# Kernel tuning notes

Hardware: AMD Instinct MI355X
Metric: run time of the kernel (lower is better)

Reference implementation:

```python
import jax, jax.numpy as jnp
import numpy as np

EMBED = 256; G = 8; NC = 6; NL = 4; NP = 13
BS = 1; NA = 900
IMG_W, IMG_H = 704.0, 256.0
LEVEL_HW = [(64, 176), (32, 88), (16, 44), (8, 22)]


def setup_inputs() -> dict:
    key = jax.random.key(0)
    ks = jax.random.split(key, 12)
    inp = {}
    inp["instance_feature"] = jax.random.normal(ks[0], (BS, NA, EMBED), jnp.float32)
    inp["anchor_embed"] = jax.random.normal(ks[1], (BS, NA, EMBED), jnp.float32)
    # key points in normalized [0,1) cube; projection matrix maps them to pixel coords
    inp["key_points"] = jax.random.uniform(ks[2], (BS, NA, NP, 3), jnp.float32)
    for i, (h, w) in enumerate(LEVEL_HW):
        inp[f"fm{i}"] = jax.random.normal(ks[3 + i], (BS, NC, EMBED, h, w), jnp.float32)
    # intrinsics-like projection: x->x*W, y->y*H, depth ~ z+0.5, plus per-camera jitter
    base = jnp.array([[IMG_W, 0.0, 0.0, 0.0],
                      [0.0, IMG_H, 0.0, 0.0],
                      [0.0, 0.0, 1.0, 0.5],
                      [0.0, 0.0, 0.0, 1.0]], jnp.float32)
    inp["projection_mat"] = base[None, None] + 0.05 * jax.random.normal(ks[7], (BS, NC, 4, 4), jnp.float32)
    inp["image_wh"] = jnp.broadcast_to(jnp.array([IMG_W, IMG_H], jnp.float32), (BS, NC, 2))
    inp["w_weights"] = 0.02 * jax.random.normal(ks[8], (EMBED, G * NC * NL * NP), jnp.float32)
    inp["b_weights"] = jnp.zeros((G * NC * NL * NP,), jnp.float32)
    inp["w_out"] = 0.02 * jax.random.normal(ks[9], (EMBED, EMBED), jnp.float32)
    inp["b_out"] = jnp.zeros((EMBED,), jnp.float32)
    return inp


def _grid_sample(fm, grid):
    # fm: (B, C, H, W); grid: (B, A, P, 2) in [-1,1]. Bilinear, zero padding,
    # align_corners=False (torch F.grid_sample defaults). Returns (B, A, P, C).
    B, C, H, W = fm.shape
    A, P = grid.shape[1], grid.shape[2]
    gx = (grid[..., 0] + 1.0) * (W * 0.5) - 0.5
    gy = (grid[..., 1] + 1.0) * (H * 0.5) - 0.5
    x0 = jnp.floor(gx); y0 = jnp.floor(gy)
    fmf = jnp.transpose(fm.reshape(B, C, H * W), (0, 2, 1))  # (B, HW, C)

    def gather(xi, yi):
        valid = (xi >= 0) & (xi <= W - 1) & (yi >= 0) & (yi <= H - 1)
        xc = jnp.clip(xi, 0, W - 1).astype(jnp.int32)
        yc = jnp.clip(yi, 0, H - 1).astype(jnp.int32)
        idx = (yc * W + xc).reshape(B, A * P, 1)
        g = jnp.take_along_axis(fmf, idx, axis=1).reshape(B, A, P, C)
        return g * valid[..., None].astype(fm.dtype)

    wx1 = gx - x0; wx0 = 1.0 - wx1
    wy1 = gy - y0; wy0 = 1.0 - wy1
    return (gather(x0, y0) * (wx0 * wy0)[..., None]
            + gather(x0 + 1.0, y0) * (wx1 * wy0)[..., None]
            + gather(x0, y0 + 1.0) * (wx0 * wy1)[..., None]
            + gather(x0 + 1.0, y0 + 1.0) * (wx1 * wy1)[..., None])


def reference(instance_feature, anchor_embed, key_points, fm0, fm1, fm2, fm3,
              projection_mat, image_wh, w_weights, b_weights, w_out, b_out):
    bs, na = instance_feature.shape[:2]
    gd = EMBED // G
    # _get_weights: softmax over (cams*levels*pts) jointly, per group
    feat = instance_feature + anchor_embed
    w = (feat @ w_weights + b_weights).reshape(bs, na, NC * NL * NP, G)
    w = jax.nn.softmax(w, axis=2).reshape(bs, na, NC, NL, NP, G)
    # feature_sampling: project 3D key points to each camera's pixel plane
    kp_h = jnp.concatenate([key_points, jnp.ones_like(key_points[..., :1])], axis=-1)
    p2 = jnp.einsum('bcij,banj->bcani', projection_mat, kp_h)  # (bs,cams,na,pts,4)
    xy = p2[..., :2] / jnp.maximum(p2[..., 2:3], 1e-5)
    grid = (xy / image_wh[:, :, None, None]) * 2.0 - 1.0
    grid = grid.reshape(bs * NC, na, NP, 2)
    # bilinear sample every pyramid level for every camera
    feats = jnp.stack([
        _grid_sample(fm.reshape(bs * NC, EMBED, fm.shape[-2], fm.shape[-1]), grid)
        for fm in (fm0, fm1, fm2, fm3)
    ], axis=0)  # (L, bs*cams, na, pts, E)
    feats = feats.reshape(NL, bs, NC, na, NP, G, gd)
    # multi_view_level_fusion: weighted sum over cams and levels, per group
    fused = jnp.einsum('baclpg,lbcapgd->bapgd', w, feats).reshape(bs, na, NP, EMBED)
    out = fused.sum(axis=2)  # sum over key points
    return out @ w_out + b_out + instance_feature  # output_proj + residual 'add'
```

## Files before the change

kernel.cpp:

```cpp
#include <hip/hip_runtime.h>
#include <hip/hip_bf16.h>
#include <hip/hip_fp16.h>
#include <cstdint>

#define EMBED 256
#define GPS 8
#define NCAM 6
#define NLVL 4
#define NPT 13
#define NANC 900
#define NSAMP (NCAM*NLVL*NPT)
#define NWCOL (GPS*NSAMP)
#define MPAD 928
#define WSTRIDE 328
#define MAXENT 320

#define FMOFF0 0
#define FMOFF1 17301504
#define FMOFF2 21626880
#define FMOFF3 22708224
#define TALL_ELEMS 22978560

typedef __attribute__((ext_vector_type(8))) short bf16x8;
typedef __attribute__((ext_vector_type(16))) float f32x16;
typedef __attribute__((ext_vector_type(8))) unsigned short ushort8_t;

__device__ __forceinline__ ushort bf16bits(float x) {
    __hip_bfloat16 h = __float2bfloat16(x);
    return *reinterpret_cast<ushort*>(&h);
}
__device__ __forceinline__ ushort h16bits(float x) {
    __half h = __float2half(x);
    return *reinterpret_cast<ushort*>(&h);
}
__device__ __forceinline__ __half2 u2h2(unsigned u) {
    union { unsigned u; __half2 h; } cv; cv.u = u; return cv.h;
}

__global__ __launch_bounds__(256) void k_prep(
        const float* __restrict__ fm0, const float* __restrict__ fm1,
        const float* __restrict__ fm2, const float* __restrict__ fm3,
        __half* __restrict__ t0, __half* __restrict__ t1,
        __half* __restrict__ t2, __half* __restrict__ t3,
        const float* __restrict__ wlin, __hip_bfloat16* __restrict__ wt,
        const float* __restrict__ inst, const float* __restrict__ anch,
        __hip_bfloat16* __restrict__ featB,
        const float* __restrict__ kp, const float* __restrict__ proj,
        float* __restrict__ pxy) {
    __shared__ ushort lds2[256 * 64];
    int b = blockIdx.x;
    int t = threadIdx.x;
    if (b < 1404) {
        const float* in; __half* outp; int HW, chunks, lb;
        if (b < 1056)      { in = fm0; outp = t0; HW = 11264; chunks = 176; lb = b; }
        else if (b < 1320) { in = fm1; outp = t1; HW = 2816;  chunks = 44;  lb = b - 1056; }
        else if (b < 1386) { in = fm2; outp = t2; HW = 704;   chunks = 11;  lb = b - 1320; }
        else               { in = fm3; outp = t3; HW = 176;   chunks = 3;   lb = b - 1386; }
        int c = lb / chunks;
        int hw0 = (lb - c * chunks) * 64;
        int q = t & 15, eg = t >> 4;
        bool vld = (hw0 + q * 4 + 3) < HW;
        const float* srcq = in + (size_t)c * EMBED * HW + hw0 + q * 4;
        float4 vals[16];
        #pragma unroll
        for (int r = 0; r < 16; r++) {
            int e = eg + r * 16;
            vals[r] = vld ? *(const float4*)(srcq + (size_t)e * HW)
                          : make_float4(0.f, 0.f, 0.f, 0.f);
        }
        #pragma unroll
        for (int r = 0; r < 16; r++) {
            int e = eg + r * 16;
            int sw = ((e >> 3) & 15) * 4;
            ushort4 u;
            u.x = h16bits(vals[r].x); u.y = h16bits(vals[r].y);
            u.z = h16bits(vals[r].z); u.w = h16bits(vals[r].w);
            *reinterpret_cast<ushort4*>(&lds2[e * 64 + ((q * 4) ^ sw)]) = u;
        }
        __syncthreads();
        ushort* outb = reinterpret_cast<ushort*>(outp) + ((size_t)c * HW + hw0) * EMBED;
        #pragma unroll
        for (int r = 0; r < 8; r++) {
            int flat = r * 2048 + t * 8;
            int hw = flat >> 8;
            int e0 = flat & 255;
            if (hw0 + hw < HW) {
                ushort8_t u;
                #pragma unroll
                for (int j = 0; j < 8; j++) {
                    int e = e0 + j;
                    int sw = ((e >> 3) & 15) * 4;
                    u[j] = lds2[e * 64 + (hw ^ sw)];
                }
                *reinterpret_cast<ushort8_t*>(outb + flat) = u;
            }
        }
    } else if (b < 1560) {
        int b1 = b - 1404;
        int kt = b1 / 39, nt = b1 - kt * 39;
        int k0 = kt * 64, n0 = nt * 64;
        int grp = t >> 6, nn = t & 63;
        #pragma unroll
        for (int r = 0; r < 16; r++) {
            int kk = grp * 16 + r;
            lds2[kk * 65 + nn] = bf16bits(wlin[(size_t)(k0 + kk) * NWCOL + n0 + nn]);
        }
        __syncthreads();
        ushort* wtb = reinterpret_cast<ushort*>(wt);
        int kk2 = t & 63;
        #pragma unroll
        for (int r = 0; r < 16; r++) {
            int nn2 = grp * 16 + r;
            wtb[(size_t)(n0 + nn2) * EMBED + k0 + kk2] = lds2[kk2 * 65 + nn2];
        }
    } else if (b < 1785) {
        int base = (b - 1560) * 1024 + t * 4;
        float4 a = *(const float4*)&inst[base];
        float4 c = *(const float4*)&anch[base];
        ushort4 r;
        r.x = bf16bits(a.x + c.x); r.y = bf16bits(a.y + c.y);
        r.z = bf16bits(a.z + c.z); r.w = bf16bits(a.w + c.w);
        *reinterpret_cast<ushort4*>(reinterpret_cast<ushort*>(featB) + base) = r;
    } else if (b < 1792) {
        int base = 900 * EMBED + (b - 1785) * 1024 + t * 4;
        ushort4 z; z.x = z.y = z.z = z.w = 0;
        *reinterpret_cast<ushort4*>(reinterpret_cast<ushort*>(featB) + base) = z;
    } else {
        int i = (b - 1792) * 256 + t;
        if (i < NANC * NCAM * NPT) {
            int a = i / (NCAM * NPT);
            int r = i - a * (NCAM * NPT);
            int c = r / NPT;
            int p = r - c * NPT;
            const float* M = proj + c * 16;
            const float* k3 = kp + ((size_t)a * NPT + p) * 3;
            float kx = k3[0], ky = k3[1], kz = k3[2];
            float X = M[0] * kx + M[1] * ky + M[2] * kz + M[3];
            float Y = M[4] * kx + M[5] * ky + M[6] * kz + M[7];
            float Z = M[8] * kx + M[9] * ky + M[10] * kz + M[11];
            float invz = 1.f / fmaxf(Z, 1e-5f);
            pxy[(size_t)i * 2 + 0] = X * invz;
            pxy[(size_t)i * 2 + 1] = Y * invz;
        }
    }
}

#define MT 29
#define NT 78
__global__ __launch_bounds__(256) void k_gemm(const __hip_bfloat16* __restrict__ featB,
                                              const __hip_bfloat16* __restrict__ wt,
                                              const float* __restrict__ blin,
                                              float* __restrict__ logits) {
    int wv = threadIdx.x >> 6, lane = threadIdx.x & 63;
    int idx = blockIdx.x * 4 + wv;
    if (idx >= MT * NT) return;
    int mt = idx % MT, nt = idx / MT;
    int m0 = mt * 32, n0 = nt * 32;
    int l31 = lane & 31;
    int khalf = (lane >> 5) * 8;
    const short* ap = reinterpret_cast<const short*>(featB) + (size_t)(m0 + l31) * EMBED + khalf;
    const short* bp = reinterpret_cast<const short*>(wt)    + (size_t)(n0 + l31) * EMBED + khalf;
    f32x16 acc = {};
    #pragma unroll 8
    for (int ki = 0; ki < 16; ki++) {
        bf16x8 a = *reinterpret_cast<const bf16x8*>(ap + ki * 16);
        bf16x8 bb = *reinterpret_cast<const bf16x8*>(bp + ki * 16);
        acc = __builtin_amdgcn_mfma_f32_32x32x16_bf16(a, bb, acc, 0, 0, 0);
    }
    float bias = blin[n0 + l31];
    int colg = n0 + l31;
    #pragma unroll
    for (int r = 0; r < 16; r++) {
        int row = (r & 3) + 8 * (r >> 2) + 4 * (lane >> 5);
        int grow = m0 + row;
        if (grow < NANC)
            logits[(size_t)grow * NWCOL + colg] = acc[r] + bias;
    }
}

__global__ __launch_bounds__(512) void k_aggregate(const __half* __restrict__ tAll,
                                                   const float* __restrict__ logits,
                                                   const float* __restrict__ pxy,
                                                   const float* __restrict__ wout,
                                                   const float* __restrict__ bout,
                                                   const float* __restrict__ inst,
                                                   float* __restrict__ out) {
    __shared__ float wT[GPS * WSTRIDE];
    __shared__ float xyS[NCAM * NPT * 2];
    __shared__ float redS[8][EMBED];
    __shared__ float pS[EMBED];
    __shared__ int4  eOff[MAXENT];
    __shared__ float4 eW[MAXENT];
    __shared__ int   eS[MAXENT];
    __shared__ int   cntS;
    int a = blockIdx.x;
    int tid = threadIdx.x;
    int wave = tid >> 6;
    int lane = tid & 63;
    if (tid == 0) cntS = 0;
    for (int j = tid; j < NWCOL; j += 512)
        wT[(j & 7) * WSTRIDE + (j >> 3)] = logits[(size_t)a * NWCOL + j];
    for (int j = tid; j < NCAM * NPT * 2; j += 512)
        xyS[j] = pxy[(size_t)a * NCAM * NPT * 2 + j];
    __syncthreads();
    {
        int g = wave;
        float m = -1e30f;
        for (int s = lane; s < NSAMP; s += 64) m = fmaxf(m, wT[g * WSTRIDE + s]);
        #pragma unroll
        for (int off = 32; off; off >>= 1) m = fmaxf(m, __shfl_xor(m, off));
        float ssum = 0.f;
        for (int s = lane; s < NSAMP; s += 64) ssum += __expf(wT[g * WSTRIDE + s] - m);
        #pragma unroll
        for (int off = 32; off; off >>= 1) ssum += __shfl_xor(ssum, off);
        float rs = 1.f / ssum;
        for (int s = lane; s < NSAMP; s += 64)
            wT[g * WSTRIDE + s] = __expf(wT[g * WSTRIDE + s] - m) * rs;
    }
    {
        bool valid = false; int4 o4; float4 w4;
        if (tid < NSAMP) {
            int c = tid / 52, rem = tid - c * 52;
            int l = rem / 13, p = rem - l * 13;
            float X = xyS[(c * NPT + p) * 2], Y = xyS[(c * NPT + p) * 2 + 1];
            int Wl = 176 >> l, Hl = 64 >> l;
            float scale = 0.25f / (float)(1 << l);
            float gx = fmaf(X, scale, -0.5f);
            float gy = fmaf(Y, scale, -0.5f);
            float x0f = floorf(gx), y0f = floorf(gy);
            float fx = gx - x0f, fy = gy - y0f;
            int x0 = (int)x0f, y0 = (int)y0f;
            int x1 = x0 + 1, y1 = y0 + 1;
            bool vx0 = (x0 >= 0) && (x0 < Wl);
            bool vx1 = (x1 >= 0) && (x1 < Wl);
            bool vy0 = (y0 >= 0) && (y0 < Hl);
            bool vy1 = (y1 >= 0) && (y1 < Hl);
            w4.x = (vx0 && vy0) ? (1.f - fx) * (1.f - fy) : 0.f;
            w4.y = (vx1 && vy0) ? fx * (1.f - fy) : 0.f;
            w4.z = (vx0 && vy1) ? (1.f - fx) * fy : 0.f;
            w4.w = (vx1 && vy1) ? fx * fy : 0.f;
            if (w4.x + w4.y + w4.z + w4.w > 0.f) {
                valid = true;
                int xc0 = min(max(x0, 0), Wl - 1), xc1 = min(max(x1, 0), Wl - 1);
                int yc0 = min(max(y0, 0), Hl - 1), yc1 = min(max(y1, 0), Hl - 1);
                const int lvlBase[4] = { FMOFF0, FMOFF1, FMOFF2, FMOFF3 };
                int cb = lvlBase[l] + c * (Wl * Hl) * EMBED;
                o4.x = cb + (yc0 * Wl + xc0) * EMBED;
                o4.y = cb + (yc0 * Wl + xc1) * EMBED;
                o4.z = cb + (yc1 * Wl + xc0) * EMBED;
                o4.w = cb + (yc1 * Wl + xc1) * EMBED;
            }
        }
        unsigned long long mask = __ballot(valid);
        int prefix = __popcll(mask & ((1ull << lane) - 1ull));
        int wcount = __popcll(mask);
        int basev = 0;
        if (lane == 0 && wcount) basev = atomicAdd(&cntS, wcount);
        basev = __shfl(basev, 0);
        if (valid) {
            int pos = basev + prefix;
            eOff[pos] = o4; eW[pos] = w4; eS[pos] = tid;
        }
    }
    __syncthreads();
    int cnt = cntS;
    int cnt_pad = (cnt + 15) & ~15;
    for (int j = cnt + tid; j < cnt_pad; j += 512) {
        eOff[j] = make_int4(0, 0, 0, 0);
        eW[j] = make_float4(0.f, 0.f, 0.f, 0.f);
        eS[j] = 0;
    }
    __syncthreads();
    int e0 = lane * 4;
    int g = lane >> 3;
    float a0 = 0.f, a1 = 0.f, a2 = 0.f, a3 = 0.f;
    auto consume = [&](const float4& w, int sIdx,
                       uint2 l0, uint2 l1, uint2 l2, uint2 l3) {
        float wg = wT[g * WSTRIDE + sIdx];
        __half2 W00 = __float2half2_rn(w.x), W01 = __float2half2_rn(w.y);
        __half2 W10 = __float2half2_rn(w.z), W11 = __float2half2_rn(w.w);
        __half2 blo = __hfma2(u2h2(l0.x), W00,
                      __hfma2(u2h2(l1.x), W01,
                      __hfma2(u2h2(l2.x), W10,
                      __hmul2(u2h2(l3.x), W11))));
        __half2 bhi = __hfma2(u2h2(l0.y), W00,
                      __hfma2(u2h2(l1.y), W01,
                      __hfma2(u2h2(l2.y), W10,
                      __hmul2(u2h2(l3.y), W11))));
        float2 flo = __half22float2(blo);
        float2 fhi = __half22float2(bhi);
        a0 = fmaf(wg, flo.x, a0);
        a1 = fmaf(wg, flo.y, a1);
        a2 = fmaf(wg, fhi.x, a2);
        a3 = fmaf(wg, fhi.y, a3);
    };
    int per = cnt_pad >> 3;
    if (per > 0) {
        int idx = wave;
        int4 oA = eOff[idx]; float4 wA = eW[idx]; int sA = eS[idx];
        uint2 vA0 = *(const uint2*)(tAll + oA.x + e0);
        uint2 vA1 = *(const uint2*)(tAll + oA.y + e0);
        uint2 vA2 = *(const uint2*)(tAll + oA.z + e0);
        uint2 vA3 = *(const uint2*)(tAll + oA.w + e0);
        for (int it = 0; it < per; it += 2) {
            int j = idx + 8;
            int4 oB = eOff[j]; float4 wB = eW[j]; int sB = eS[j];
            uint2 vB0 = *(const uint2*)(tAll + oB.x + e0);
            uint2 vB1 = *(const uint2*)(tAll + oB.y + e0);
            uint2 vB2 = *(const uint2*)(tAll + oB.z + e0);
            uint2 vB3 = *(const uint2*)(tAll + oB.w + e0);
            consume(wA, sA, vA0, vA1, vA2, vA3);
            idx = j + 8;
            if (it + 2 < per) {
                oA = eOff[idx]; wA = eW[idx]; sA = eS[idx];
                vA0 = *(const uint2*)(tAll + oA.x + e0);
                vA1 = *(const uint2*)(tAll + oA.y + e0);
                vA2 = *(const uint2*)(tAll + oA.z + e0);
                vA3 = *(const uint2*)(tAll + oA.w + e0);
            }
            consume(wB, sB, vB0, vB1, vB2, vB3);
        }
    }
    redS[wave][e0 + 0] = a0; redS[wave][e0 + 1] = a1;
    redS[wave][e0 + 2] = a2; redS[wave][e0 + 3] = a3;
    __syncthreads();
    int col = tid & 255;
    int kh = tid >> 8;
    if (kh == 0) {
        float s = redS[0][col] + redS[1][col] + redS[2][col] + redS[3][col]
                + redS[4][col] + redS[5][col] + redS[6][col] + redS[7][col];
        redS[0][col] = s;
    }
    __syncthreads();
    float acc = 0.f;
    int kbase = kh * 128;
    #pragma unroll 8
    for (int k = 0; k < 128; k++)
        acc = fmaf(redS[0][kbase + k], wout[(size_t)(kbase + k) * EMBED + col], acc);
    if (kh == 1) pS[col] = acc;
    __syncthreads();
    if (kh == 0)
        out[(size_t)a * EMBED + col] = acc + pS[col] + bout[col] + inst[(size_t)a * EMBED + col];
}

extern "C" void kernel_launch(void* const* d_in, const int* in_sizes, int n_in,
                              void* d_out, int out_size, void* d_ws, size_t ws_size,
                              hipStream_t stream) {
    const float* inst = (const float*)d_in[0];
    const float* anch = (const float*)d_in[1];
    const float* kp   = (const float*)d_in[2];
    const float* fm0  = (const float*)d_in[3];
    const float* fm1  = (const float*)d_in[4];
    const float* fm2  = (const float*)d_in[5];
    const float* fm3  = (const float*)d_in[6];
    const float* proj = (const float*)d_in[7];
    const float* wlin = (const float*)d_in[9];
    const float* blin = (const float*)d_in[10];
    const float* wout = (const float*)d_in[11];
    const float* bout = (const float*)d_in[12];
    float* out = (float*)d_out;

    char* ws = (char*)d_ws;
    size_t off = 0;
    auto alloc = [&](size_t bytes) -> void* {
        void* p = ws + off;
        off = (off + bytes + 255) & ~(size_t)255;
        return p;
    };
    __half* tAll = (__half*)alloc((size_t)TALL_ELEMS * 2);
    __half* t0 = tAll + FMOFF0;
    __half* t1 = tAll + FMOFF1;
    __half* t2 = tAll + FMOFF2;
    __half* t3 = tAll + FMOFF3;
    __hip_bfloat16* wt    = (__hip_bfloat16*)alloc((size_t)NWCOL * EMBED * 2);
    __hip_bfloat16* featB = (__hip_bfloat16*)alloc((size_t)MPAD * EMBED * 2);
    float* logits = (float*)alloc((size_t)NANC * NWCOL * 4);
    float* pxy    = (float*)alloc((size_t)NANC * NCAM * NPT * 2 * 4);

    k_prep<<<dim3(2067), 256, 0, stream>>>(fm0, fm1, fm2, fm3, t0, t1, t2, t3,
                                           wlin, wt, inst, anch, featB, kp, proj, pxy);
    k_gemm<<<dim3((MT * NT + 3) / 4), 256, 0, stream>>>(featB, wt, blin, logits);
    k_aggregate<<<dim3(NANC), 512, 0, stream>>>(tAll, logits, pxy,
                                                wout, bout, inst, out);
}
```

Baseline: 217.1 us.

## Store transposed feature maps as FP8 instead of FP16

The prep kernel now packs each channel-last feature map element into FP8 (e4m3 via cvt_pk_fp8) instead of half precision, halving the transposed buffer size. The aggregate kernel loads 4 bytes per lane per corner and unpacks them to fp32 with cvt_pk_f32_fp8, then folds the bilinear and softmax weights in fp32. The aim is to cut global write traffic in prep and gather bandwidth in aggregate. The cost is a large loss of precision in the sampled features, which may hurt accuracy against a float32 reference, plus a changed LDS swizzle and larger entry padding.

```diff
diff --git a/kernel.cpp b/kernel.cpp
--- a/kernel.cpp
+++ b/kernel.cpp
@@ -13,45 +13,38 @@
 #define NWCOL (GPS*NSAMP)
 #define MPAD 928
 #define WSTRIDE 328
-#define MAXENT 320
+#define MAXENT 352
 
 #define FMOFF0 0
 #define FMOFF1 17301504
 #define FMOFF2 21626880
 #define FMOFF3 22708224
-#define TALL_ELEMS 22978560
+#define TALL_BYTES 22978560
 
 typedef __attribute__((ext_vector_type(8))) short bf16x8;
 typedef __attribute__((ext_vector_type(16))) float f32x16;
-typedef __attribute__((ext_vector_type(8))) unsigned short ushort8_t;
+typedef __attribute__((ext_vector_type(2))) float v2f;
 
 __device__ __forceinline__ ushort bf16bits(float x) {
     __hip_bfloat16 h = __float2bfloat16(x);
     return *reinterpret_cast<ushort*>(&h);
 }
-__device__ __forceinline__ ushort h16bits(float x) {
-    __half h = __float2half(x);
-    return *reinterpret_cast<ushort*>(&h);
-}
-__device__ __forceinline__ __half2 u2h2(unsigned u) {
-    union { unsigned u; __half2 h; } cv; cv.u = u; return cv.h;
-}
 
 __global__ __launch_bounds__(256) void k_prep(
         const float* __restrict__ fm0, const float* __restrict__ fm1,
         const float* __restrict__ fm2, const float* __restrict__ fm3,
-        __half* __restrict__ t0, __half* __restrict__ t1,
-        __half* __restrict__ t2, __half* __restrict__ t3,
+        unsigned char* __restrict__ t0, unsigned char* __restrict__ t1,
+        unsigned char* __restrict__ t2, unsigned char* __restrict__ t3,
         const float* __restrict__ wlin, __hip_bfloat16* __restrict__ wt,
         const float* __restrict__ inst, const float* __restrict__ anch,
         __hip_bfloat16* __restrict__ featB,
         const float* __restrict__ kp, const float* __restrict__ proj,
         float* __restrict__ pxy) {
-    __shared__ ushort lds2[256 * 64];
+    __shared__ ushort lds2[128 * 64];
     int b = blockIdx.x;
     int t = threadIdx.x;
     if (b < 1404) {
-        const float* in; __half* outp; int HW, chunks, lb;
+        const float* in; unsigned char* outp; int HW, chunks, lb;
         if (b < 1056)      { in = fm0; outp = t0; HW = 11264; chunks = 176; lb = b; }
         else if (b < 1320) { in = fm1; outp = t1; HW = 2816;  chunks = 44;  lb = b - 1056; }
         else if (b < 1386) { in = fm2; outp = t2; HW = 704;   chunks = 11;  lb = b - 1320; }
@@ -64,35 +57,40 @@
         float4 vals[16];
         #pragma unroll
         for (int r = 0; r < 16; r++) {
-            int e = eg + r * 16;
+            int e = 2 * eg + (r & 1) + 32 * (r >> 1);
             vals[r] = vld ? *(const float4*)(srcq + (size_t)e * HW)
                           : make_float4(0.f, 0.f, 0.f, 0.f);
         }
         #pragma unroll
-        for (int r = 0; r < 16; r++) {
-            int e = eg + r * 16;
-            int sw = ((e >> 3) & 15) * 4;
-            ushort4 u;
-            u.x = h16bits(vals[r].x); u.y = h16bits(vals[r].y);
-            u.z = h16bits(vals[r].z); u.w = h16bits(vals[r].w);
-            *reinterpret_cast<ushort4*>(&lds2[e * 64 + ((q * 4) ^ sw)]) = u;
+        for (int rp = 0; rp < 8; rp++) {
+            int ep = eg + 16 * rp;
+            int s2 = (ep >> 1) & 62;
+            float4 va = vals[2 * rp], vb = vals[2 * rp + 1];
+            uint p0 = (uint)__builtin_amdgcn_cvt_pk_fp8_f32(va.x, vb.x, 0, false) & 0xffff;
+            uint p1 = (uint)__builtin_amdgcn_cvt_pk_fp8_f32(va.y, vb.y, 0, false) & 0xffff;
+            uint p2 = (uint)__builtin_amdgcn_cvt_pk_fp8_f32(va.z, vb.z, 0, false) & 0xffff;
+            uint p3 = (uint)__builtin_amdgcn_cvt_pk_fp8_f32(va.w, vb.w, 0, false) & 0xffff;
+            int col01 = (q * 4) ^ s2;
+            int col23 = (q * 4 + 2) ^ s2;
+            *reinterpret_cast<uint*>(&lds2[ep * 64 + col01]) = p0 | (p1 << 16);
+            *reinterpret_cast<uint*>(&lds2[ep * 64 + col23]) = p2 | (p3 << 16);
         }
         __syncthreads();
-        ushort* outb = reinterpret_cast<ushort*>(outp) + ((size_t)c * HW + hw0) * EMBED;
+        ushort* outb = reinterpret_cast<ushort*>(outp) + ((size_t)c * HW + hw0) * 128;
         #pragma unroll
         for (int r = 0; r < 8; r++) {
             int flat = r * 2048 + t * 8;
             int hw = flat >> 8;
-            int e0 = flat & 255;
+            int ep0 = (flat & 255) >> 1;
             if (hw0 + hw < HW) {
-                ushort8_t u;
+                ushort4 u;
                 #pragma unroll
-                for (int j = 0; j < 8; j++) {
-                    int e = e0 + j;
-                    int sw = ((e >> 3) & 15) * 4;
-                    u[j] = lds2[e * 64 + (hw ^ sw)];
+                for (int j = 0; j < 4; j++) {
+                    int ep = ep0 + j;
+                    int s2 = (ep >> 1) & 62;
+                    u[j] = lds2[ep * 64 + (hw ^ s2)];
                 }
-                *reinterpret_cast<ushort8_t*>(outb + flat) = u;
+                *reinterpret_cast<ushort4*>(outb + flat / 2) = u;
             }
         }
     } else if (b < 1560) {
@@ -178,7 +176,7 @@
     }
 }
 
-__global__ __launch_bounds__(512) void k_aggregate(const __half* __restrict__ tAll,
+__global__ __launch_bounds__(512) void k_aggregate(const unsigned char* __restrict__ tAll,
                                                    const float* __restrict__ logits,
                                                    const float* __restrict__ pxy,
                                                    const float* __restrict__ wout,
@@ -265,7 +263,7 @@
     __syncthreads();
     int cnt = cntS;
     int cnt_pad = (cnt + 15) & ~15;
-    for (int j = cnt + tid; j < cnt_pad; j += 512) {
+    for (int j = cnt + tid; j < cnt_pad + 16; j += 512) {
         eOff[j] = make_int4(0, 0, 0, 0);
         eW[j] = make_float4(0.f, 0.f, 0.f, 0.f);
         eS[j] = 0;
@@ -275,48 +273,45 @@
     int g = lane >> 3;
     float a0 = 0.f, a1 = 0.f, a2 = 0.f, a3 = 0.f;
     auto consume = [&](const float4& w, int sIdx,
-                       uint2 l0, uint2 l1, uint2 l2, uint2 l3) {
+                       uint c00, uint c01, uint c10, uint c11) {
         float wg = wT[g * WSTRIDE + sIdx];
-        __half2 W00 = __float2half2_rn(w.x), W01 = __float2half2_rn(w.y);
-        __half2 W10 = __float2half2_rn(w.z), W11 = __float2half2_rn(w.w);
-        __half2 blo = __hfma2(u2h2(l0.x), W00,
-                      __hfma2(u2h2(l1.x), W01,
-                      __hfma2(u2h2(l2.x), W10,
-                      __hmul2(u2h2(l3.x), W11))));
-        __half2 bhi = __hfma2(u2h2(l0.y), W00,
-                      __hfma2(u2h2(l1.y), W01,
-                      __hfma2(u2h2(l2.y), W10,
-                      __hmul2(u2h2(l3.y), W11))));
-        float2 flo = __half22float2(blo);
-        float2 fhi = __half22float2(bhi);
-        a0 = fmaf(wg, flo.x, a0);
-        a1 = fmaf(wg, flo.y, a1);
-        a2 = fmaf(wg, fhi.x, a2);
-        a3 = fmaf(wg, fhi.y, a3);
+        float wwx = wg * w.x, wwy = wg * w.y, wwz = wg * w.z, www = wg * w.w;
+        v2f l00 = __builtin_amdgcn_cvt_pk_f32_fp8(c00, false);
+        v2f h00 = __builtin_amdgcn_cvt_pk_f32_fp8(c00, true);
+        v2f l01 = __builtin_amdgcn_cvt_pk_f32_fp8(c01, false);
+        v2f h01 = __builtin_amdgcn_cvt_pk_f32_fp8(c01, true);
+        v2f l10 = __builtin_amdgcn_cvt_pk_f32_fp8(c10, false);
+        v2f h10 = __builtin_amdgcn_cvt_pk_f32_fp8(c10, true);
+        v2f l11 = __builtin_amdgcn_cvt_pk_f32_fp8(c11, false);
+        v2f h11 = __builtin_amdgcn_cvt_pk_f32_fp8(c11, true);
+        a0 = fmaf(wwx, l00.x, fmaf(wwy, l01.x, fmaf(wwz, l10.x, fmaf(www, l11.x, a0))));
+        a1 = fmaf(wwx, l00.y, fmaf(wwy, l01.y, fmaf(wwz, l10.y, fmaf(www, l11.y, a1))));
+        a2 = fmaf(wwx, h00.x, fmaf(wwy, h01.x, fmaf(wwz, h10.x, fmaf(www, h11.x, a2))));
+        a3 = fmaf(wwx, h00.y, fmaf(wwy, h01.y, fmaf(wwz, h10.y, fmaf(www, h11.y, a3))));
     };
     int per = cnt_pad >> 3;
     if (per > 0) {
         int idx = wave;
         int4 oA = eOff[idx]; float4 wA = eW[idx]; int sA = eS[idx];
-        uint2 vA0 = *(const uint2*)(tAll + oA.x + e0);
-        uint2 vA1 = *(const uint2*)(tAll + oA.y + e0);
-        uint2 vA2 = *(const uint2*)(tAll + oA.z + e0);
-        uint2 vA3 = *(const uint2*)(tAll + oA.w + e0);
+        uint vA0 = *(const uint*)(tAll + oA.x + e0);
+        uint vA1 = *(const uint*)(tAll + oA.y + e0);
+        uint vA2 = *(const uint*)(tAll + oA.z + e0);
+        uint vA3 = *(const uint*)(tAll + oA.w + e0);
         for (int it = 0; it < per; it += 2) {
             int j = idx + 8;
             int4 oB = eOff[j]; float4 wB = eW[j]; int sB = eS[j];
-            uint2 vB0 = *(const uint2*)(tAll + oB.x + e0);
-            uint2 vB1 = *(const uint2*)(tAll + oB.y + e0);
-            uint2 vB2 = *(const uint2*)(tAll + oB.z + e0);
-            uint2 vB3 = *(const uint2*)(tAll + oB.w + e0);
+            uint vB0 = *(const uint*)(tAll + oB.x + e0);
+            uint vB1 = *(const uint*)(tAll + oB.y + e0);
+            uint vB2 = *(const uint*)(tAll + oB.z + e0);
+            uint vB3 = *(const uint*)(tAll + oB.w + e0);
             consume(wA, sA, vA0, vA1, vA2, vA3);
             idx = j + 8;
             if (it + 2 < per) {
                 oA = eOff[idx]; wA = eW[idx]; sA = eS[idx];
-                vA0 = *(const uint2*)(tAll + oA.x + e0);
-                vA1 = *(const uint2*)(tAll + oA.y + e0);
-                vA2 = *(const uint2*)(tAll + oA.z + e0);
-                vA3 = *(const uint2*)(tAll + oA.w + e0);
+                vA0 = *(const uint*)(tAll + oA.x + e0);
+                vA1 = *(const uint*)(tAll + oA.y + e0);
+                vA2 = *(const uint*)(tAll + oA.z + e0);
+                vA3 = *(const uint*)(tAll + oA.w + e0);
             }
             consume(wB, sB, vB0, vB1, vB2, vB3);
         }
@@ -367,11 +362,11 @@
         off = (off + bytes + 255) & ~(size_t)255;
         return p;
     };
-    __half* tAll = (__half*)alloc((size_t)TALL_ELEMS * 2);
-    __half* t0 = tAll + FMOFF0;
-    __half* t1 = tAll + FMOFF1;
-    __half* t2 = tAll + FMOFF2;
-    __half* t3 = tAll + FMOFF3;
+    unsigned char* tAll = (unsigned char*)alloc((size_t)TALL_BYTES);
+    unsigned char* t0 = tAll + FMOFF0;
+    unsigned char* t1 = tAll + FMOFF1;
+    unsigned char* t2 = tAll + FMOFF2;
+    unsigned char* t3 = tAll + FMOFF3;
     __hip_bfloat16* wt    = (__hip_bfloat16*)alloc((size_t)NWCOL * EMBED * 2);
     __hip_bfloat16* featB = (__hip_bfloat16*)alloc((size_t)MPAD * EMBED * 2);
     float* logits = (float*)alloc((size_t)NANC * NWCOL * 4);
```

Result: faster. 194.7 us (-10.3%).
